# Kernel optimization log

Measured on AMD Instinct MI355X. Metric: run time of the kernel, lower is better.

## Reference

```python
import jax, jax.numpy as jnp
import numpy as np

N, F_IN, F_OUT = 8192, 256, 128
ALPHA = 0.2  # LeakyReLU negative slope
NEG_INF = -9e15


def setup_inputs() -> dict:
    key = jax.random.key(0)
    k1, k2, k3, k4 = jax.random.split(key, 4)
    h = jax.random.normal(k1, (N, F_IN), dtype=jnp.float32)
    adj = jax.random.randint(k2, (N, N), 0, 2, dtype=jnp.int32)
    # Xavier-uniform-like init (gain=1.414)
    lim_w = 1.414 * np.sqrt(6.0 / (F_IN + F_OUT))
    W = jax.random.uniform(k3, (F_IN, F_OUT), dtype=jnp.float32, minval=-lim_w, maxval=lim_w)
    lim_a = 1.414 * np.sqrt(6.0 / (2 * F_OUT + 1))
    a = jax.random.uniform(k4, (2 * F_OUT, 1), dtype=jnp.float32, minval=-lim_a, maxval=lim_a)
    return {"h": h, "adj": adj, "W": W, "a": a}


def reference(h, adj, W, a):
    # Wh: [N, F_OUT]
    Wh = h @ W
    f_out = W.shape[1]
    # The torch code builds an [N, N, 2F] concat tensor; mathematically
    # e_ij = leakyrelu(a1 . Wh_i + a2 . Wh_j), so compute via two projections.
    a1 = a[:f_out, 0]   # [F_OUT]
    a2 = a[f_out:, 0]   # [F_OUT]
    f1 = Wh @ a1        # [N]
    f2 = Wh @ a2        # [N]
    e = jax.nn.leaky_relu(f1[:, None] + f2[None, :], negative_slope=ALPHA)  # [N, N]
    e = jnp.where(adj > 0, e, NEG_INF)
    attention = jax.nn.softmax(e, axis=1)  # [N, N]; dropout p=0 (eval mode)
    h_prime = attention @ Wh               # [N, F_OUT]
    return jax.nn.elu(h_prime)
```

## Files before the change

### kernel.cpp

```cpp
#include <hip/hip_runtime.h>
#include <hip/hip_bf16.h>
#include <math.h>

typedef short short8 __attribute__((ext_vector_type(8)));
typedef float f32x4 __attribute__((ext_vector_type(4)));
typedef int i32x4 __attribute__((ext_vector_type(4)));

#define NN 8192
#define FIN 256
#define FOUT 128
#define LRELU_A 0.2f
#define L2E 1.44269504088896f

__device__ __forceinline__ short f2bf(float x) {
    unsigned u = __builtin_bit_cast(unsigned, x);
    unsigned r = (u + 0x7FFFu + ((u >> 16) & 1u)) >> 16;
    return (short)r;
}

__device__ __forceinline__ short f2bf_fast(float x) {
    return __builtin_bit_cast(short, __float2bfloat16(x));
}

__device__ __forceinline__ float bf2f(short s) {
    return __builtin_bit_cast(float, (int)((unsigned short)s) << 16);
}

__global__ __launch_bounds__(256) void k_prep(const float* __restrict__ h,
                                              const float* __restrict__ W,
                                              const float* __restrict__ a,
                                              const int* __restrict__ adj,
                                              short* __restrict__ WhT,
                                              float* __restrict__ f1,
                                              float* __restrict__ f2,
                                              unsigned* __restrict__ packed) {
    __shared__ float hs[8][FIN];
    __shared__ unsigned char nib[2048];
    const int tid = threadIdx.x;
    const int bid = blockIdx.x;

    if (bid >= NN / 8) {
        const int row = bid - NN / 8;
        const i32x4* base = (const i32x4*)(adj + (size_t)row * NN);
        #pragma unroll
        for (int q = 0; q < 8; ++q) {
            int idx = q * 256 + tid;
            i32x4 v = __builtin_nontemporal_load(base + idx);
            unsigned b = (unsigned)(v.x & 1)        | ((unsigned)(v.y & 1) << 1) |
                         ((unsigned)(v.z & 1) << 2) | ((unsigned)(v.w & 1) << 3);
            nib[idx] = (unsigned char)b;
        }
        __syncthreads();
        unsigned long long n8 = *(const unsigned long long*)&nib[tid * 8];
        unsigned w = 0;
        #pragma unroll
        for (int j = 0; j < 8; ++j)
            w |= ((unsigned)((n8 >> (8 * j)) & 0xFull)) << (4 * j);
        packed[(size_t)row * (NN / 32) + tid] = w;
        return;
    }

    const int swz = (bid & 7) * 128 + (bid >> 3);
    const int r0 = swz * 8;
    #pragma unroll
    for (int i = 0; i < 2; ++i) {
        int f4 = tid + 256 * i;
        int row = f4 >> 6;
        int k4 = (f4 & 63) << 2;
        *(float4*)&hs[row][k4] = *(const float4*)(h + (size_t)(r0 + row) * FIN + k4);
    }
    __syncthreads();
    const int c4 = (tid & 31) * 4;
    const int row = tid >> 5;
    float acc0 = 0.f, acc1 = 0.f, acc2 = 0.f, acc3 = 0.f;
    #pragma unroll 4
    for (int k = 0; k < FIN; ++k) {
        float hv = hs[row][k];
        float4 w4 = *(const float4*)(W + (size_t)k * FOUT + c4);
        acc0 = fmaf(hv, w4.x, acc0);
        acc1 = fmaf(hv, w4.y, acc1);
        acc2 = fmaf(hv, w4.z, acc2);
        acc3 = fmaf(hv, w4.w, acc3);
    }
    const int wr = r0 + row;

    __syncthreads();
    short (*tws)[8] = (short (*)[8])hs;
    tws[c4 + 0][row] = f2bf(acc0);
    tws[c4 + 1][row] = f2bf(acc1);
    tws[c4 + 2][row] = f2bf(acc2);
    tws[c4 + 3][row] = f2bf(acc3);

    float4 a1v = *(const float4*)(a + c4);
    float4 a2v = *(const float4*)(a + FOUT + c4);
    float p1 = acc0 * a1v.x + acc1 * a1v.y + acc2 * a1v.z + acc3 * a1v.w;
    float p2 = acc0 * a2v.x + acc1 * a2v.y + acc2 * a2v.z + acc3 * a2v.w;
    #pragma unroll
    for (int m = 1; m <= 16; m <<= 1) {
        p1 += __shfl_xor(p1, m, 64);
        p2 += __shfl_xor(p2, m, 64);
    }
    if ((tid & 31) == 0) {
        f1[wr] = p1;
        f2[wr] = p2;
    }

    __syncthreads();
    if (tid < FOUT)
        *(short8*)(WhT + (size_t)tid * NN + r0) = *(const short8*)tws[tid];
}

__device__ __forceinline__ void gat_body(const short* __restrict__ lrd, unsigned m8,
                                         float4 fa, float4 fb,
                                         float c1, float c2,
                                         f32x4 acc[9], short8 ones) {
    short8 b0 = *(const short8*)(lrd + 0 * 1024);
    short8 b1 = *(const short8*)(lrd + 1 * 1024);
    short8 b2 = *(const short8*)(lrd + 2 * 1024);
    short8 b3 = *(const short8*)(lrd + 3 * 1024);
    short8 b4 = *(const short8*)(lrd + 4 * 1024);
    short8 b5 = *(const short8*)(lrd + 5 * 1024);
    short8 b6 = *(const short8*)(lrd + 6 * 1024);
    short8 b7 = *(const short8*)(lrd + 7 * 1024);

    float fv[8] = {fa.x, fa.y, fa.z, fa.w, fb.x, fb.y, fb.z, fb.w};
    short8 af;
    #pragma unroll
    for (int i = 0; i < 8; ++i) {
        float u = fmaf(L2E, fv[i], c1);
        float v = fmaf(LRELU_A * L2E, fv[i], c2);
        float p = __builtin_amdgcn_exp2f(fmaxf(u, v));
        p = (m8 & (1u << i)) ? p : 0.0f;
        af[i] = f2bf_fast(p);
    }
    acc[0] = __builtin_amdgcn_mfma_f32_16x16x32_bf16(af, b0, acc[0], 0, 0, 0);
    acc[1] = __builtin_amdgcn_mfma_f32_16x16x32_bf16(af, b1, acc[1], 0, 0, 0);
    acc[2] = __builtin_amdgcn_mfma_f32_16x16x32_bf16(af, b2, acc[2], 0, 0, 0);
    acc[3] = __builtin_amdgcn_mfma_f32_16x16x32_bf16(af, b3, acc[3], 0, 0, 0);
    acc[4] = __builtin_amdgcn_mfma_f32_16x16x32_bf16(af, b4, acc[4], 0, 0, 0);
    acc[5] = __builtin_amdgcn_mfma_f32_16x16x32_bf16(af, b5, acc[5], 0, 0, 0);
    acc[6] = __builtin_amdgcn_mfma_f32_16x16x32_bf16(af, b6, acc[6], 0, 0, 0);
    acc[7] = __builtin_amdgcn_mfma_f32_16x16x32_bf16(af, b7, acc[7], 0, 0, 0);
    acc[8] = __builtin_amdgcn_mfma_f32_16x16x32_bf16(af, ones, acc[8], 0, 0, 0);
}

#define GAT_STEP(KOFF, MC, LRD0, LRD1, BUFW)                                       \
    {                                                                              \
        const int koff_ = (KOFF);                                                  \
        float4 fa0 = *(const float4*)(lf2 + koff_);                                \
        float4 fb0 = *(const float4*)(lf2 + koff_ + 4);                            \
        float4 fa1 = *(const float4*)(lf2 + koff_ + 32);                           \
        float4 fb1 = *(const float4*)(lf2 + koff_ + 36);                           \
        unsigned m0 = (MC.x >> mshift) & 0xffu;                                    \
        unsigned m1 = (MC.y >> mshift) & 0xffu;                                    \
        const int kpm_ = (koff_ + 128 < kchunk) ? koff_ + 128 : 0;                 \
        MC = *(const uint2*)(pkrow + (kpm_ >> 5));                                 \
        const int kst_ = (koff_ + 64 < kchunk) ? koff_ + 64 : 0;                   \
        short8 r0 = *(const short8*)(g00 + kst_);                                  \
        short8 r1 = *(const short8*)(g01 + kst_);                                  \
        short8 r2 = *(const short8*)(g10 + kst_);                                  \
        short8 r3 = *(const short8*)(g11 + kst_);                                  \
        gat_body(LRD0, m0, fa0, fb0, c1, c2, acc, ones);                           \
        gat_body(LRD1, m1, fa1, fb1, c1, c2, acc, ones);                           \
        *(short8*)((BUFW) + d00) = r0;                                             \
        *(short8*)((BUFW) + d01) = r1;                                             \
        *(short8*)((BUFW) + d10) = r2;                                             \
        *(short8*)((BUFW) + d11) = r3;                                             \
        asm volatile("s_waitcnt lgkmcnt(0)" ::: "memory");                         \
        __builtin_amdgcn_s_barrier();                                              \
    }

__global__ __launch_bounds__(256, 4) void k_attn(const unsigned* __restrict__ packed,
                                                 const short* __restrict__ WhT,
                                                 const float* __restrict__ f1,
                                                 const float* __restrict__ f2,
                                                 short* __restrict__ numb,
                                                 float* __restrict__ denb,
                                                 int kchunk, int nsplit) {
    __shared__ __align__(16) short ldsW[2][8192];
    __shared__ __align__(16) float ldsF2[2048];
    const int tid = threadIdx.x;
    const int lane = tid & 63;
    const int wave = tid >> 6;
    const int split = blockIdx.x & (nsplit - 1);
    const int rt = blockIdx.x / nsplit;
    const int rowbase = rt * 64 + wave * 16;
    const int col = lane & 15;
    const int kg = lane >> 4;
    const int arow = rowbase + col;

    float gm = -3.4e38f;
    for (int i = tid * 4; i < NN; i += 1024) {
        float4 v = *(const float4*)(f2 + i);
        gm = fmaxf(fmaxf(gm, fmaxf(v.x, v.y)), fmaxf(v.z, v.w));
    }
    #pragma unroll
    for (int s = 1; s <= 32; s <<= 1) gm = fmaxf(gm, __shfl_xor(gm, s, 64));
    if (lane == 0) ldsF2[wave] = gm;
    __syncthreads();
    gm = fmaxf(fmaxf(ldsF2[0], ldsF2[1]), fmaxf(ldsF2[2], ldsF2[3]));
    __syncthreads();

    const float f1r = f1[arow];
    const float t0v = f1r + gm;
    const float mhat = fmaxf(t0v, LRELU_A * t0v);
    const float mh2 = mhat * L2E;
    const float c1 = fmaf(f1r, L2E, -mh2);
    const float c2 = fmaf(LRELU_A * f1r, L2E, -mh2);

    const short8 ones = {0x3F80, 0x3F80, 0x3F80, 0x3F80,
                         0x3F80, 0x3F80, 0x3F80, 0x3F80};

    const int kbase0 = split * kchunk;
    const unsigned* pkrow = packed + (size_t)arow * (NN / 32) + (kbase0 >> 5);
    const int mshift = kg * 8;
    const float* lf2 = ldsF2 + kg * 8;

    const int srow = wave * 32 + (lane >> 2);
    const int sx = srow & 7;
    const short* gsb = WhT + (size_t)srow * NN + kbase0 + (lane & 3) * 8;
    const short* g00 = gsb;
    const short* g01 = gsb + 32;
    const short* g10 = gsb + (size_t)16 * NN;
    const short* g11 = gsb + (size_t)16 * NN + 32;
    const int d00 = srow * 64        + ((((lane & 3) + 0) ^ sx) * 8);
    const int d01 = srow * 64        + ((((lane & 3) + 4) ^ sx) * 8);
    const int d10 = (srow + 16) * 64 + ((((lane & 3) + 0) ^ sx) * 8);
    const int d11 = (srow + 16) * 64 + ((((lane & 3) + 4) ^ sx) * 8);
    short* buf0 = &ldsW[0][0];
    short* buf1 = &ldsW[1][0];

    const short* lrdE0 = &ldsW[0][col * 64 + ((kg ^ (col & 7)) * 8)];
    const short* lrdE1 = &ldsW[0][col * 64 + (((kg ^ (col & 7)) * 8) ^ 32)];
    const short* lrdO0 = lrdE0 + 8192;
    const short* lrdO1 = lrdE1 + 8192;

    f32x4 acc[9] = {};

    for (int i = tid * 4; i < kchunk; i += 1024)
        *(float4*)&ldsF2[i] = *(const float4*)(f2 + kbase0 + i);
    {
        short8 r0 = *(const short8*)(g00);
        short8 r1 = *(const short8*)(g01);
        short8 r2 = *(const short8*)(g10);
        short8 r3 = *(const short8*)(g11);
        *(short8*)(buf0 + d00) = r0;
        *(short8*)(buf0 + d01) = r1;
        *(short8*)(buf0 + d10) = r2;
        *(short8*)(buf0 + d11) = r3;
    }
    uint2 mA = *(const uint2*)(pkrow);
    uint2 mB = *(const uint2*)(pkrow + 2);
    asm volatile("s_waitcnt lgkmcnt(0)" ::: "memory");
    __builtin_amdgcn_s_barrier();

    for (int koff = 0; koff < kchunk; koff += 128) {
        GAT_STEP(koff,      mA, lrdE0, lrdE1, buf1);
        GAT_STEP(koff + 64, mB, lrdO0, lrdO1, buf0);
    }

    const int rsub = (lane >> 4) * 4;
    if (col == 0) {
        #pragma unroll
        for (int r = 0; r < 4; ++r)
            __builtin_nontemporal_store(acc[8][r],
                &denb[(size_t)split * NN + rowbase + rsub + r]);
    }
    short* np = numb + ((size_t)split * NN + rowbase) * FOUT;
    #pragma unroll
    for (int t = 0; t < 8; ++t) {
        #pragma unroll
        for (int r = 0; r < 4; ++r) {
            __builtin_nontemporal_store(f2bf_fast(acc[t][r]),
                &np[(size_t)(rsub + r) * FOUT + t * 16 + col]);
        }
    }
}

__global__ __launch_bounds__(256) void k_final(const short* __restrict__ numb,
                                               const float* __restrict__ denb,
                                               float* __restrict__ out,
                                               int splitk) {
    const int idx8 = blockIdx.x * 256 + threadIdx.x;
    const int row = idx8 >> 4;
    const int cg = (idx8 & 15) * 8;
    float s[8] = {0.f, 0.f, 0.f, 0.f, 0.f, 0.f, 0.f, 0.f};
    float d = 0.0f;
    for (int sp = 0; sp < splitk; ++sp) {
        short8 v = __builtin_nontemporal_load(
            (const short8*)&numb[((size_t)sp * NN + row) * FOUT + cg]);
        #pragma unroll
        for (int j = 0; j < 8; ++j) s[j] += bf2f(v[j]);
        d += denb[(size_t)sp * NN + row];
    }
    const float rd = 1.0f / d;
    f32x4 o0, o1;
    #pragma unroll
    for (int j = 0; j < 4; ++j) {
        float v = s[j] * rd;
        o0[j] = v > 0.0f ? v : expm1f(v);
    }
    #pragma unroll
    for (int j = 0; j < 4; ++j) {
        float v = s[4 + j] * rd;
        o1[j] = v > 0.0f ? v : expm1f(v);
    }
    float* op = out + (size_t)row * FOUT + cg;
    __builtin_nontemporal_store(o0, (f32x4*)op);
    __builtin_nontemporal_store(o1, (f32x4*)(op + 4));
}

extern "C" void kernel_launch(void* const* d_in, const int* in_sizes, int n_in,
                              void* d_out, int out_size, void* d_ws, size_t ws_size,
                              hipStream_t stream) {
    const float* h = (const float*)d_in[0];
    const int* adj = (const int*)d_in[1];
    const float* W = (const float*)d_in[2];
    const float* a = (const float*)d_in[3];
    float* out = (float*)d_out;

    char* ws = (char*)d_ws;
    size_t off = 0;
    auto alloc = [&](size_t nbytes) {
        char* p = ws + off;
        off = (off + nbytes + 255) & ~(size_t)255;
        return p;
    };
    short* WhT     = (short*)alloc((size_t)FOUT * NN * 2);
    float* f1      = (float*)alloc(NN * 4);
    float* f2      = (float*)alloc(NN * 4);
    unsigned* pkd  = (unsigned*)alloc((size_t)NN * (NN / 32) * 4);

    int splitk = 8;
    while (splitk > 1 &&
           off + (size_t)splitk * ((size_t)NN * FOUT * 2 + NN * 4 + 512) > ws_size)
        splitk >>= 1;
    short* numb = (short*)alloc((size_t)splitk * NN * FOUT * 2);
    float* denb = (float*)alloc((size_t)splitk * NN * 4);
    const int kchunk = NN / splitk;

    k_prep<<<NN / 8 + NN, 256, 0, stream>>>(h, W, a, adj, WhT, f1, f2, pkd);
    k_attn<<<(NN / 64) * splitk, 256, 0, stream>>>(pkd, WhT, f1, f2, numb, denb,
                                                   kchunk, splitk);
    k_final<<<NN * FOUT / 8 / 256, 256, 0, stream>>>(numb, denb, out, splitk);
}
```

Measured before the change: 116.4 us.

## Fuse adjacency bit-packing into attention kernel, drop separate packed mask pass

```diff
diff --git a/kernel.cpp b/kernel.cpp
--- a/kernel.cpp
+++ b/kernel.cpp
@@ -26,39 +26,22 @@
     return __builtin_bit_cast(float, (int)((unsigned short)s) << 16);
 }
 
+__device__ __forceinline__ unsigned pack8(i32x4 a, i32x4 b) {
+    return (unsigned)(a.x & 1)        | ((unsigned)(a.y & 1) << 1) |
+           ((unsigned)(a.z & 1) << 2) | ((unsigned)(a.w & 1) << 3) |
+           ((unsigned)(b.x & 1) << 4) | ((unsigned)(b.y & 1) << 5) |
+           ((unsigned)(b.z & 1) << 6) | ((unsigned)(b.w & 1) << 7);
+}
+
 __global__ __launch_bounds__(256) void k_prep(const float* __restrict__ h,
                                               const float* __restrict__ W,
                                               const float* __restrict__ a,
-                                              const int* __restrict__ adj,
                                               short* __restrict__ WhT,
                                               float* __restrict__ f1,
-                                              float* __restrict__ f2,
-                                              unsigned* __restrict__ packed) {
+                                              float* __restrict__ f2) {
     __shared__ float hs[8][FIN];
-    __shared__ unsigned char nib[2048];
     const int tid = threadIdx.x;
     const int bid = blockIdx.x;
-
-    if (bid >= NN / 8) {
-        const int row = bid - NN / 8;
-        const i32x4* base = (const i32x4*)(adj + (size_t)row * NN);
-        #pragma unroll
-        for (int q = 0; q < 8; ++q) {
-            int idx = q * 256 + tid;
-            i32x4 v = __builtin_nontemporal_load(base + idx);
-            unsigned b = (unsigned)(v.x & 1)        | ((unsigned)(v.y & 1) << 1) |
-                         ((unsigned)(v.z & 1) << 2) | ((unsigned)(v.w & 1) << 3);
-            nib[idx] = (unsigned char)b;
-        }
-        __syncthreads();
-        unsigned long long n8 = *(const unsigned long long*)&nib[tid * 8];
-        unsigned w = 0;
-        #pragma unroll
-        for (int j = 0; j < 8; ++j)
-            w |= ((unsigned)((n8 >> (8 * j)) & 0xFull)) << (4 * j);
-        packed[(size_t)row * (NN / 32) + tid] = w;
-        return;
-    }
 
     const int swz = (bid & 7) * 128 + (bid >> 3);
     const int r0 = swz * 8;
@@ -144,24 +127,28 @@
     acc[8] = __builtin_amdgcn_mfma_f32_16x16x32_bf16(af, ones, acc[8], 0, 0, 0);
 }
 
-#define GAT_STEP(KOFF, MC, LRD0, LRD1, BUFW)                                       \
+#define GAT_STEP(KOFF, LRD0, LRD1, BUFW, MCUR, MNXT)                               \
     {                                                                              \
         const int koff_ = (KOFF);                                                  \
+        unsigned m0 = (MCUR)[cofs0];                                               \
+        unsigned m1 = (MCUR)[cofs1];                                               \
         float4 fa0 = *(const float4*)(lf2 + koff_);                                \
         float4 fb0 = *(const float4*)(lf2 + koff_ + 4);                            \
         float4 fa1 = *(const float4*)(lf2 + koff_ + 32);                           \
         float4 fb1 = *(const float4*)(lf2 + koff_ + 36);                           \
-        unsigned m0 = (MC.x >> mshift) & 0xffu;                                    \
-        unsigned m1 = (MC.y >> mshift) & 0xffu;                                    \
-        const int kpm_ = (koff_ + 128 < kchunk) ? koff_ + 128 : 0;                 \
-        MC = *(const uint2*)(pkrow + (kpm_ >> 5));                                 \
         const int kst_ = (koff_ + 64 < kchunk) ? koff_ + 64 : 0;                   \
+        i32x4 xa0 = *(const i32x4*)(adjp0 + kst_);                                 \
+        i32x4 xa1 = *(const i32x4*)(adjp0 + kst_ + 4);                             \
+        i32x4 xb0 = *(const i32x4*)(adjp1 + kst_);                                 \
+        i32x4 xb1 = *(const i32x4*)(adjp1 + kst_ + 4);                             \
         short8 r0 = *(const short8*)(g00 + kst_);                                  \
         short8 r1 = *(const short8*)(g01 + kst_);                                  \
         short8 r2 = *(const short8*)(g10 + kst_);                                  \
         short8 r3 = *(const short8*)(g11 + kst_);                                  \
         gat_body(LRD0, m0, fa0, fb0, c1, c2, acc, ones);                           \
         gat_body(LRD1, m1, fa1, fb1, c1, c2, acc, ones);                           \
+        (MNXT)[pofs0] = (unsigned char)pack8(xa0, xa1);                            \
+        (MNXT)[pofs1] = (unsigned char)pack8(xb0, xb1);                            \
         *(short8*)((BUFW) + d00) = r0;                                             \
         *(short8*)((BUFW) + d01) = r1;                                             \
         *(short8*)((BUFW) + d10) = r2;                                             \
@@ -170,7 +157,7 @@
         __builtin_amdgcn_s_barrier();                                              \
     }
 
-__global__ __launch_bounds__(256, 4) void k_attn(const unsigned* __restrict__ packed,
+__global__ __launch_bounds__(256, 4) void k_attn(const int* __restrict__ adj,
                                                  const short* __restrict__ WhT,
                                                  const float* __restrict__ f1,
                                                  const float* __restrict__ f2,
@@ -178,13 +165,15 @@
                                                  float* __restrict__ denb,
                                                  int kchunk, int nsplit) {
     __shared__ __align__(16) short ldsW[2][8192];
-    __shared__ __align__(16) float ldsF2[2048];
+    __shared__ __align__(16) float ldsF2[1024];
+    __shared__ __align__(8) unsigned char mbuf[2][64][8];
     const int tid = threadIdx.x;
     const int lane = tid & 63;
     const int wave = tid >> 6;
     const int split = blockIdx.x & (nsplit - 1);
     const int rt = blockIdx.x / nsplit;
-    const int rowbase = rt * 64 + wave * 16;
+    const int rowbase0 = rt * 64;
+    const int rowbase = rowbase0 + wave * 16;
     const int col = lane & 15;
     const int kg = lane >> 4;
     const int arow = rowbase + col;
@@ -212,9 +201,19 @@
                          0x3F80, 0x3F80, 0x3F80, 0x3F80};
 
     const int kbase0 = split * kchunk;
-    const unsigned* pkrow = packed + (size_t)arow * (NN / 32) + (kbase0 >> 5);
-    const int mshift = kg * 8;
     const float* lf2 = ldsF2 + kg * 8;
+
+    const int prow = tid >> 3;
+    const int pcq = tid & 7;
+    const int* adjp0 = adj + (size_t)(rowbase0 + prow) * NN + kbase0 + pcq * 8;
+    const int* adjp1 = adjp0 + (size_t)32 * NN;
+    const int pofs0 = prow * 8 + pcq;
+    const int pofs1 = (32 + prow) * 8 + pcq;
+    const int rowc = wave * 16 + col;
+    const int cofs0 = rowc * 8 + kg;
+    const int cofs1 = rowc * 8 + 4 + kg;
+    unsigned char* mb0 = &mbuf[0][0][0];
+    unsigned char* mb1 = &mbuf[1][0][0];
 
     const int srow = wave * 32 + (lane >> 2);
     const int sx = srow & 7;
@@ -248,15 +247,19 @@
         *(short8*)(buf0 + d01) = r1;
         *(short8*)(buf0 + d10) = r2;
         *(short8*)(buf0 + d11) = r3;
-    }
-    uint2 mA = *(const uint2*)(pkrow);
-    uint2 mB = *(const uint2*)(pkrow + 2);
+        i32x4 xa0 = *(const i32x4*)(adjp0);
+        i32x4 xa1 = *(const i32x4*)(adjp0 + 4);
+        i32x4 xb0 = *(const i32x4*)(adjp1);
+        i32x4 xb1 = *(const i32x4*)(adjp1 + 4);
+        mb0[pofs0] = (unsigned char)pack8(xa0, xa1);
+        mb0[pofs1] = (unsigned char)pack8(xb0, xb1);
+    }
     asm volatile("s_waitcnt lgkmcnt(0)" ::: "memory");
     __builtin_amdgcn_s_barrier();
 
     for (int koff = 0; koff < kchunk; koff += 128) {
-        GAT_STEP(koff,      mA, lrdE0, lrdE1, buf1);
-        GAT_STEP(koff + 64, mB, lrdO0, lrdO1, buf0);
+        GAT_STEP(koff,      lrdE0, lrdE1, buf1, mb0, mb1);
+        GAT_STEP(koff + 64, lrdO0, lrdO1, buf0, mb1, mb0);
     }
 
     const int rsub = (lane >> 4) * 4;
@@ -326,21 +329,17 @@
         off = (off + nbytes + 255) & ~(size_t)255;
         return p;
     };
-    short* WhT     = (short*)alloc((size_t)FOUT * NN * 2);
-    float* f1      = (float*)alloc(NN * 4);
-    float* f2      = (float*)alloc(NN * 4);
-    unsigned* pkd  = (unsigned*)alloc((size_t)NN * (NN / 32) * 4);
-
-    int splitk = 8;
-    while (splitk > 1 &&
-           off + (size_t)splitk * ((size_t)NN * FOUT * 2 + NN * 4 + 512) > ws_size)
-        splitk >>= 1;
+    short* WhT = (short*)alloc((size_t)FOUT * NN * 2);
+    float* f1  = (float*)alloc(NN * 4);
+    float* f2  = (float*)alloc(NN * 4);
+
+    const int splitk = 8;
     short* numb = (short*)alloc((size_t)splitk * NN * FOUT * 2);
     float* denb = (float*)alloc((size_t)splitk * NN * 4);
     const int kchunk = NN / splitk;
 
-    k_prep<<<NN / 8 + NN, 256, 0, stream>>>(h, W, a, adj, WhT, f1, f2, pkd);
-    k_attn<<<(NN / 64) * splitk, 256, 0, stream>>>(pkd, WhT, f1, f2, numb, denb,
+    k_prep<<<NN / 8, 256, 0, stream>>>(h, W, a, WhT, f1, f2);
+    k_attn<<<(NN / 64) * splitk, 256, 0, stream>>>(adj, WhT, f1, f2, numb, denb,
                                                    kchunk, splitk);
     k_final<<<NN * FOUT / 8 / 256, 256, 0, stream>>>(numb, denb, out, splitk);
 }
```

New measurement: 139.8 us. +20.1%, slower.
